# Kernel tuning notes

Hardware: AMD Instinct MI355X
Metric: run time of the kernel (lower is better)

## Reference

```python
import jax, jax.numpy as jnp
import numpy as np

B, C, L = 2, 512, 4096
HEADS, KV_HEADS, DIM_HEAD = 8, 2, 64
ROTARY_DIM = 32  # int(64 * 0.5), even
ROPE_THETA = 10000.0
SCALE = DIM_HEAD ** -0.5


def _rotate_half(x):
    # pairs (x0, x1) -> (-x1, x0), interleaved layout
    x = x.reshape(*x.shape[:-1], x.shape[-1] // 2, 2)
    x1, x2 = x[..., 0], x[..., 1]
    return jnp.stack([-x2, x1], axis=-1).reshape(*x.shape[:-2], x.shape[-2] * 2)


def _rope_sin_cos(seq_len, rotary_dim, theta, dtype):
    positions = jnp.arange(seq_len, dtype=dtype)
    half = rotary_dim // 2
    inv_freq = theta ** (-2.0 * jnp.arange(half, dtype=dtype) / rotary_dim)
    sinusoid = positions[:, None] * inv_freq[None, :]          # (L, half)
    sin = jnp.repeat(jnp.sin(sinusoid), 2, axis=-1)            # (L, rotary_dim) interleaved
    cos = jnp.repeat(jnp.cos(sinusoid), 2, axis=-1)
    return sin[None, None], cos[None, None]                    # (1,1,L,rotary_dim)


def setup_inputs() -> dict:
    key = jax.random.key(0)
    kx, kq, kkv, ko = jax.random.split(key, 4)
    s = 0.02
    return {
        "x": jax.random.normal(kx, (B, C, L), dtype=jnp.float32),
        "Wq": jax.random.normal(kq, (HEADS * DIM_HEAD, C), dtype=jnp.float32) * s,
        "Wkv": jax.random.normal(kkv, (2 * KV_HEADS * DIM_HEAD, C), dtype=jnp.float32) * s,
        "Wo": jax.random.normal(ko, (C, HEADS * DIM_HEAD), dtype=jnp.float32) * s,
    }


def reference(x, Wq, Wkv, Wo):
    b, c, l = x.shape
    x_t = jnp.swapaxes(x, 1, 2)                                 # (B, L, C)
    q = x_t @ Wq.T                                              # (B, L, H*dh)
    kv = x_t @ Wkv.T                                            # (B, L, KVH*2*dh)
    q = q.reshape(b, l, HEADS, DIM_HEAD).transpose(0, 2, 1, 3)  # (B, H, L, dh)
    kv = kv.reshape(b, l, KV_HEADS, 2 * DIM_HEAD).transpose(0, 2, 1, 3)
    k, v = jnp.split(kv, 2, axis=-1)                            # (B, KVH, L, dh) each

    sin, cos = _rope_sin_cos(l, ROTARY_DIM, ROPE_THETA, x.dtype)
    q_rot, q_pass = q[..., :ROTARY_DIM], q[..., ROTARY_DIM:]
    k_rot, k_pass = k[..., :ROTARY_DIM], k[..., ROTARY_DIM:]
    q_rot = q_rot * cos + _rotate_half(q_rot) * sin
    k_rot = k_rot * cos + _rotate_half(k_rot) * sin
    q = jnp.concatenate([q_rot, q_pass], axis=-1)
    k = jnp.concatenate([k_rot, k_pass], axis=-1)

    rep = HEADS // KV_HEADS
    k = jnp.repeat(k, rep, axis=1)                              # (B, H, L, dh)
    v = jnp.repeat(v, rep, axis=1)

    q = q * SCALE
    attn = jnp.einsum('bhid,bhjd->bhij', q, k)                  # (B, H, L, L)
    attn = jax.nn.softmax(attn, axis=-1)
    out = jnp.einsum('bhij,bhjd->bhid', attn, v)                # (B, H, L, dh)
    out = out.transpose(0, 2, 1, 3).reshape(b, l, HEADS * DIM_HEAD)
    out = out @ Wo.T                                            # (B, L, C)
    return jnp.swapaxes(out, 1, 2)                              # (B, C, L)
```

## Files before the change

kernel.cpp:

```cpp
#include <hip/hip_runtime.h>

using f16   = _Float16;
using f16x2 = __attribute__((ext_vector_type(2))) f16;
using f16x4 = __attribute__((ext_vector_type(4))) f16;
using f16x8 = __attribute__((ext_vector_type(8))) f16;
using f32x4 = __attribute__((ext_vector_type(4))) float;

#define L_ 4096
#define C_ 512

static __device__ __forceinline__ float fast_exp2(float x) {
#if __has_builtin(__builtin_amdgcn_exp2f)
  return __builtin_amdgcn_exp2f(x);
#else
  float r; asm("v_exp_f32 %0, %1" : "=v"(r) : "v"(x)); return r;
#endif
}

static __device__ __forceinline__ f16x2 pk2(float a, float b) {
  return __builtin_bit_cast(f16x2, __builtin_amdgcn_cvt_pkrtz(a, b));
}

static __device__ __forceinline__ void gl16(const char* g, char* l) {
  __builtin_amdgcn_global_load_lds(
      (const __attribute__((address_space(1))) unsigned int*)g,
      (__attribute__((address_space(3))) unsigned int*)l, 16, 0, 0);
}

#define WS_SC    0u
#define WS_WQKV  524288u
#define WS_WO    1310720u
#define WS_Q     1835008u
#define WS_K     10223616u
#define WS_VT    12320768u
#define WS_ATT   14417920u
#define WS_OP    22806528u
#define WS_LS2   56360960u
#define WS_END2  56885248u

__global__ __launch_bounds__(256) void prep_kernel(
    const float* __restrict__ Wq, const float* __restrict__ Wkv,
    const float* __restrict__ Wo,
    f16* __restrict__ wqkv, f16* __restrict__ wo16, float2* __restrict__ sc) {
  int t = blockIdx.x * 256 + threadIdx.x;
  if (t < 98304) {
    int idx = t * 4;
    float4 v = (idx < 262144) ? *(const float4*)(Wq + idx)
                              : *(const float4*)(Wkv + (idx - 262144));
    f16x4 o = {(f16)v.x, (f16)v.y, (f16)v.z, (f16)v.w};
    *(f16x4*)(wqkv + idx) = o;
  } else if (t < 163840) {
    int idx = (t - 98304) * 4;
    float4 v = *(const float4*)(Wo + idx);
    f16x4 o = {(f16)v.x, (f16)v.y, (f16)v.z, (f16)v.w};
    *(f16x4*)(wo16 + idx) = o;
  } else if (t < 229376) {
    int e = t - 163840;
    int l = e >> 4, p = e & 15;
    float invf = exp2f(-(float)p * (13.287712379549449f / 16.0f));
    float ang = (float)l * invf;
    sc[e] = make_float2(sinf(ang), cosf(ang));
  }
}

__global__ __launch_bounds__(256) void qkv_kernel(
    const float* __restrict__ x, const f16* __restrict__ wqkv,
    const float2* __restrict__ sc,
    f16* __restrict__ Qo, f16* __restrict__ Ko, f16* __restrict__ Vto) {
  __shared__ __align__(16) f16 xt[32 * 512];
  char* xl = (char*)xt;
  int bid = blockIdx.x;
  int b   = bid / 384;
  int rem = bid % 384;
  int ot  = rem >> 7;
  int lt  = rem & 127;
  int wave = threadIdx.x >> 6, lane = threadIdx.x & 63;
  int lo = lane & 15, hi = lane >> 4;
  int obase = ot * 256 + wave * 64;
  int lbase = lt * 32;
  const float* xb = x + (size_t)b * C_ * L_;

  {
    int l  = threadIdx.x & 31;
    int cg = threadIdx.x >> 5;
#pragma unroll
    for (int p = 0; p < 16; ++p) {
      int c4 = (p * 8 + cg) * 4;
      float v0 = xb[(size_t)(c4 + 0) * L_ + lbase + l];
      float v1 = xb[(size_t)(c4 + 1) * L_ + lbase + l];
      float v2 = xb[(size_t)(c4 + 2) * L_ + lbase + l];
      float v3 = xb[(size_t)(c4 + 3) * L_ + lbase + l];
      f16x2 p01 = pk2(v0, v1), p23 = pk2(v2, v3);
      f16x4 w = {p01[0], p01[1], p23[0], p23[1]};
      int col = (c4 * 2) ^ ((l & 7) * 16);
      *(f16x4*)(xl + l * 1024 + col) = w;
    }
  }
  __syncthreads();

  f32x4 acc[4][2] = {};
  for (int kc = 0; kc < 512; kc += 32) {
    f16x8 aw[4];
#pragma unroll
    for (int oc = 0; oc < 4; ++oc)
      aw[oc] = *(const f16x8*)(wqkv + (obase + oc * 16 + lo) * 512 + kc + hi * 8);
#pragma unroll
    for (int lc = 0; lc < 2; ++lc) {
      int row = lc * 16 + lo;
      f16x8 bx = *(const f16x8*)(xl + row * 1024 + (((kc + hi * 8) * 2) ^ ((row & 7) * 16)));
#pragma unroll
      for (int oc = 0; oc < 4; ++oc)
        acc[oc][lc] = __builtin_amdgcn_mfma_f32_16x16x32_f16(aw[oc], bx, acc[oc][lc], 0, 0, 0);
    }
  }

  bool is_q = obase < 512;
  int  og   = obase - 512;
  int  kvh  = is_q ? 0 : (og >> 7);
  bool is_v = (!is_q) && ((og & 127) == 64);
  int  h    = obase >> 6;
  const float QSCALE = 0.125f * 1.44269504088896340736f;

#pragma unroll
  for (int oc = 0; oc < 4; ++oc) {
#pragma unroll
    for (int lc = 0; lc < 2; ++lc) {
      f32x4 v = acc[oc][lc];
      int l = lbase + lc * 16 + lo;
      int d = oc * 16 + hi * 4;
      if (!is_v && oc < 2) {
        int p0 = d >> 1;
        float2 s0 = sc[l * 16 + p0];
        float2 s1 = sc[l * 16 + p0 + 1];
        float a0 = v[0], a1 = v[1], a2 = v[2], a3 = v[3];
        v[0] = a0 * s0.y - a1 * s0.x;
        v[1] = a1 * s0.y + a0 * s0.x;
        v[2] = a2 * s1.y - a3 * s1.x;
        v[3] = a3 * s1.y + a2 * s1.x;
      }
      if (is_q) {
        f16x4 st = {(f16)(v[0] * QSCALE), (f16)(v[1] * QSCALE),
                    (f16)(v[2] * QSCALE), (f16)(v[3] * QSCALE)};
        *(f16x4*)(Qo + (((size_t)b * 8 + h) * L_ + l) * 64 + d) = st;
      } else if (!is_v) {
        f16x4 st = {(f16)v[0], (f16)v[1], (f16)v[2], (f16)v[3]};
        int t = l >> 6, r = l & 63;
        int u = (d >> 3) ^ (r & 7);
        int w = (hi & 1) * 8;
        char* Kb = (char*)Ko + (size_t)(b * 2 + kvh) * (L_ * 128);
        *(f16x4*)(Kb + (size_t)t * 8192 + r * 128 + u * 16 + w) = st;
      } else {
        int t = l >> 6, kk = l & 63;
        int m = kk >> 3, i8 = kk & 7;
        int ca = (m >> 2) * 64 + ((2 * m) & 3) * 16 + ((m >> 1) & 1) * 8;
        int bcol = ca + (i8 < 4 ? 2 * i8 : 8 + 2 * i8);
        char* Vb = (char*)Vto + (size_t)(b * 2 + kvh) * (L_ * 128);
#pragma unroll
        for (int i = 0; i < 4; ++i) {
          int rv = d + i;
          *(f16*)(Vb + (size_t)t * 8192 + rv * 128 + (bcol ^ ((rv & 7) << 4))) = (f16)v[i];
        }
      }
    }
  }
}

template <int SPLIT>
__global__ __launch_bounds__(512) void attn_kernel(
    const f16* __restrict__ Qi, const f16* __restrict__ Ki,
    const f16* __restrict__ Vti, f16* __restrict__ att,
    f16* __restrict__ opart, float* __restrict__ lsews) {
  __shared__ __align__(16) char smem[2][16384];
  int bid  = blockIdx.x;
  int half = (SPLIT > 1) ? (bid >> 7) : 0;
  int rem7 = bid & 127;
  int b   = rem7 >> 6;
  int rr  = rem7 & 63;
  int h   = rr >> 3;
  int qt  = rr & 7;
  int tid  = threadIdx.x;
  int wave = tid >> 6, lane = tid & 63;
  int lo = lane & 15, hi = lane >> 4;
  int kvh = h >> 2;
  const f16*  Qp   = Qi + ((size_t)(b * 8 + h) * L_) * 64;
  const char* Ksrc = (const char*)Ki  + (size_t)(b * 2 + kvh) * (L_ * 128)
                     + (size_t)half * (L_ / SPLIT) * 128;
  const char* Vsrc = (const char*)Vti + (size_t)(b * 2 + kvh) * (L_ * 128)
                     + (size_t)half * (L_ / SPLIT) * 128;

  int lqb = qt * 512 + wave * 64;
  f16x8 qf[4][2];
#pragma unroll
  for (int qi = 0; qi < 4; ++qi)
#pragma unroll
    for (int hf = 0; hf < 2; ++hf)
      qf[qi][hf] = *(const f16x8*)(Qp + (size_t)(lqb + qi * 16 + lo) * 64 + hf * 32 + hi * 8);

  int c0 = tid;
#define STAGE(t, base_) do {                                           \
    gl16(Ksrc + (size_t)(t) * 8192 + c0 * 16, (char*)(base_) + c0 * 16); \
    gl16(Vsrc + (size_t)(t) * 8192 + c0 * 16, (char*)(base_) + 8192 + c0 * 16); \
  } while (0)

  f32x4 oacc[4][4] = {};
  f32x4 lse[4] = {};
  const f16x8 ones8 = {(f16)1.f, (f16)1.f, (f16)1.f, (f16)1.f,
                       (f16)1.f, (f16)1.f, (f16)1.f, (f16)1.f};
  int swz = (lo & 7) << 4;

#define COMPUTE(buf_) do {                                                          \
    const char* kb = (const char*)(buf_);                                           \
    const char* vb = kb + 8192;                                                     \
    _Pragma("unroll")                                                               \
    for (int jp = 0; jp < 2; ++jp) {                                                \
      f32x4 s[2][4] = {};                                                           \
      __builtin_amdgcn_s_setprio(1);                                                \
      _Pragma("unroll")                                                             \
      for (int jj = 0; jj < 2; ++jj) {                                              \
        int j = jp * 2 + jj;                                                        \
        f16x8 ka0 = *(const f16x8*)(kb + (j * 16 + lo) * 128 + ((hi * 16) ^ swz));  \
        f16x8 ka1 = *(const f16x8*)(kb + (j * 16 + lo) * 128 + ((64 + hi * 16) ^ swz)); \
        _Pragma("unroll")                                                           \
        for (int qi = 0; qi < 4; ++qi) {                                            \
          s[jj][qi] = __builtin_amdgcn_mfma_f32_16x16x32_f16(ka0, qf[qi][0], s[jj][qi], 0, 0, 0); \
          s[jj][qi] = __builtin_amdgcn_mfma_f32_16x16x32_f16(ka1, qf[qi][1], s[jj][qi], 0, 0, 0); \
        }                                                                           \
      }                                                                             \
      __builtin_amdgcn_s_setprio(0);                                                \
      f16x8 pc[4];                                                                  \
      _Pragma("unroll")                                                             \
      for (int qi = 0; qi < 4; ++qi) {                                              \
        f16x2 a0 = pk2(fast_exp2(s[0][qi][0]), fast_exp2(s[0][qi][1]));             \
        f16x2 a1 = pk2(fast_exp2(s[0][qi][2]), fast_exp2(s[0][qi][3]));             \
        f16x2 b0 = pk2(fast_exp2(s[1][qi][0]), fast_exp2(s[1][qi][1]));             \
        f16x2 b1 = pk2(fast_exp2(s[1][qi][2]), fast_exp2(s[1][qi][3]));             \
        f16x4 l4 = __builtin_shufflevector(a0, a1, 0, 1, 2, 3);                     \
        f16x4 h4 = __builtin_shufflevector(b0, b1, 0, 1, 2, 3);                     \
        pc[qi] = __builtin_shufflevector(l4, h4, 0, 1, 2, 3, 4, 5, 6, 7);           \
      }                                                                             \
      __builtin_amdgcn_s_setprio(1);                                                \
      _Pragma("unroll")                                                             \
      for (int dc = 0; dc < 4; ++dc) {                                              \
        f16x8 vv = *(const f16x8*)(vb + (dc * 16 + lo) * 128 + ((jp * 64 + hi * 16) ^ swz)); \
        _Pragma("unroll")                                                           \
        for (int qi = 0; qi < 4; ++qi)                                              \
          oacc[dc][qi] = __builtin_amdgcn_mfma_f32_16x16x32_f16(vv, pc[qi], oacc[dc][qi], 0, 0, 0); \
      }                                                                             \
      _Pragma("unroll")                                                             \
      for (int qi = 0; qi < 4; ++qi)                                                \
        lse[qi] = __builtin_amdgcn_mfma_f32_16x16x32_f16(ones8, pc[qi], lse[qi], 0, 0, 0); \
      __builtin_amdgcn_s_setprio(0);                                                \
    }                                                                               \
  } while (0)

  const int NT = 64 / SPLIT;
  STAGE(0, smem[0]);
  __syncthreads();

  for (int t = 0; t < NT; ++t) {
    if (t + 1 < NT) STAGE(t + 1, smem[(t + 1) & 1]);
    COMPUTE(smem[t & 1]);
    __syncthreads();
  }

#pragma unroll
  for (int qi = 0; qi < 4; ++qi) {
    int lq = lqb + qi * 16 + lo;
    if constexpr (SPLIT > 1) {
      size_t obase = (((size_t)(half * 2 + b) * 8 + h) * L_ + lq) * 64;
#pragma unroll
      for (int dc = 0; dc < 4; ++dc) {
        f16x4 st;
#pragma unroll
        for (int i = 0; i < 4; ++i) st[i] = (f16)oacc[dc][qi][i];
        *(f16x4*)(opart + obase + dc * 16 + hi * 4) = st;
      }
      if (hi == 0)
        lsews[((size_t)(half * 2 + b) * 8 + h) * L_ + lq] = lse[qi][0];
    } else {
      float inv = 1.f / lse[qi][0];
#pragma unroll
      for (int dc = 0; dc < 4; ++dc) {
        f16x4 st;
#pragma unroll
        for (int i = 0; i < 4; ++i) st[i] = (f16)(oacc[dc][qi][i] * inv);
        *(f16x4*)(att + ((size_t)b * L_ + lq) * 512 + h * 64 + dc * 16 + hi * 4) = st;
      }
    }
  }
#undef STAGE
#undef COMPUTE
}

template <int SPLIT>
__global__ __launch_bounds__(256) void combine_kernel(
    const f16* __restrict__ opart, const float* __restrict__ lsews,
    f16* __restrict__ att) {
  int t = blockIdx.x * 256 + threadIdx.x;
  int d4 = t & 15;
  int lq = (t >> 4) & 4095;
  int h  = (t >> 16) & 7;
  int b  = t >> 19;
  const size_t HS  = (size_t)2 * 8 * 4096 * 64;
  const size_t LSS = (size_t)2 * 8 * 4096;
  size_t base  = (((size_t)b * 8 + h) * 4096 + lq) * 64 + d4 * 4;
  size_t lbase = ((size_t)b * 8 + h) * 4096 + lq;
  float o[4] = {};
  float ls = 0.f;
#pragma unroll
  for (int s = 0; s < SPLIT; ++s) {
    f16x4 op = *(const f16x4*)(opart + s * HS + base);
#pragma unroll
    for (int i = 0; i < 4; ++i) o[i] += (float)op[i];
    ls += lsews[s * LSS + lbase];
  }
  float inv = 1.f / ls;
  f16x4 st;
#pragma unroll
  for (int i = 0; i < 4; ++i) st[i] = (f16)(o[i] * inv);
  *(f16x4*)(att + ((size_t)b * 4096 + lq) * 512 + h * 64 + d4 * 4) = st;
}

__global__ __launch_bounds__(256) void oproj_kernel(
    const f16* __restrict__ att, const f16* __restrict__ wo16,
    float* __restrict__ out) {
  int bid = blockIdx.x;
  int b   = bid / 256;
  int rem = bid % 256;
  int ct  = rem >> 7;
  int lt  = rem & 127;
  int wave = threadIdx.x >> 6, lane = threadIdx.x & 63;
  int lo = lane & 15, hi = lane >> 4;
  int cobase = ct * 256 + wave * 64;
  int lbase  = lt * 32;
  const f16* ab = att + (size_t)b * L_ * 512;

  f32x4 acc[4][2] = {};
  for (int kc = 0; kc < 512; kc += 32) {
    f16x8 aw[4];
#pragma unroll
    for (int cc = 0; cc < 4; ++cc)
      aw[cc] = *(const f16x8*)(wo16 + (cobase + cc * 16 + lo) * 512 + kc + hi * 8);
#pragma unroll
    for (int lc = 0; lc < 2; ++lc) {
      f16x8 bx = *(const f16x8*)(ab + (size_t)(lbase + lc * 16 + lo) * 512 + kc + hi * 8);
#pragma unroll
      for (int cc = 0; cc < 4; ++cc)
        acc[cc][lc] = __builtin_amdgcn_mfma_f32_16x16x32_f16(aw[cc], bx, acc[cc][lc], 0, 0, 0);
    }
  }
  float* ob = out + (size_t)b * C_ * L_;
#pragma unroll
  for (int cc = 0; cc < 4; ++cc)
#pragma unroll
    for (int lc = 0; lc < 2; ++lc) {
      int l = lbase + lc * 16 + lo;
#pragma unroll
      for (int i = 0; i < 4; ++i) {
        int co = cobase + cc * 16 + hi * 4 + i;
        ob[(size_t)co * L_ + l] = acc[cc][lc][i];
      }
    }
}

extern "C" void kernel_launch(void* const* d_in, const int* in_sizes, int n_in,
                              void* d_out, int out_size, void* d_ws, size_t ws_size,
                              hipStream_t stream) {
  const float* x   = (const float*)d_in[0];
  const float* Wq  = (const float*)d_in[1];
  const float* Wkv = (const float*)d_in[2];
  const float* Wo  = (const float*)d_in[3];
  char* ws = (char*)d_ws;
  float2* sc  = (float2*)(ws + WS_SC);
  f16* wqkv   = (f16*)(ws + WS_WQKV);
  f16* wo16   = (f16*)(ws + WS_WO);
  f16* Qb     = (f16*)(ws + WS_Q);
  f16* Kb     = (f16*)(ws + WS_K);
  f16* Vtb    = (f16*)(ws + WS_VT);
  f16* attb   = (f16*)(ws + WS_ATT);
  f16* opb    = (f16*)(ws + WS_OP);
  float* lsb  = (float*)(ws + WS_LS2);

  prep_kernel<<<1024, 256, 0, stream>>>(Wq, Wkv, Wo, wqkv, wo16, sc);
  qkv_kernel<<<768, 256, 0, stream>>>(x, wqkv, sc, Qb, Kb, Vtb);
  if (ws_size >= (size_t)WS_END2) {
    attn_kernel<2><<<256, 512, 0, stream>>>(Qb, Kb, Vtb, attb, opb, lsb);
    combine_kernel<2><<<4096, 256, 0, stream>>>(opb, lsb, attb);
  } else {
    attn_kernel<1><<<128, 512, 0, stream>>>(Qb, Kb, Vtb, attb, opb, lsb);
  }
  oproj_kernel<<<512, 256, 0, stream>>>(attb, wo16, (float*)d_out);
}
```

Baseline: 141.7 us.

## Fuse split-KV combine into output projection kernel

Replaces the separate combine kernel and output-projection kernel with one kernel. It merges the two attention partial outputs, normalises them by the summed LSE and stages the tile in swizzled LDS, then runs the Wo GEMM over both output-channel halves. This drops one launch and the write and reread of the intermediate attention buffer. In exchange each block now does the work of two projection tiles, so the grid halves to 256 blocks, and it uses 32KB of LDS per block, which may lower occupancy.

Measured after the change: 133.0 us. 1.07x faster.

```diff
diff --git a/kernel.cpp b/kernel.cpp
--- a/kernel.cpp
+++ b/kernel.cpp
@@ -292,33 +292,78 @@
 #undef COMPUTE
 }
 
-template <int SPLIT>
-__global__ __launch_bounds__(256) void combine_kernel(
+__global__ __launch_bounds__(256) void oproj_fused_kernel(
     const f16* __restrict__ opart, const float* __restrict__ lsews,
-    f16* __restrict__ att) {
-  int t = blockIdx.x * 256 + threadIdx.x;
-  int d4 = t & 15;
-  int lq = (t >> 4) & 4095;
-  int h  = (t >> 16) & 7;
-  int b  = t >> 19;
+    const f16* __restrict__ wo16, float* __restrict__ out) {
+  __shared__ __align__(16) f16 bt[32 * 512];
+  __shared__ float linv[32][8];
+  char* bl = (char*)bt;
+  int bid = blockIdx.x;
+  int b   = bid >> 7;
+  int lt  = bid & 127;
+  int lbase = lt * 32;
+  int tid  = threadIdx.x;
+  int wave = tid >> 6, lane = tid & 63;
+  int lo = lane & 15, hi = lane >> 4;
   const size_t HS  = (size_t)2 * 8 * 4096 * 64;
   const size_t LSS = (size_t)2 * 8 * 4096;
-  size_t base  = (((size_t)b * 8 + h) * 4096 + lq) * 64 + d4 * 4;
-  size_t lbase = ((size_t)b * 8 + h) * 4096 + lq;
-  float o[4] = {};
-  float ls = 0.f;
-#pragma unroll
-  for (int s = 0; s < SPLIT; ++s) {
-    f16x4 op = *(const f16x4*)(opart + s * HS + base);
-#pragma unroll
-    for (int i = 0; i < 4; ++i) o[i] += (float)op[i];
-    ls += lsews[s * LSS + lbase];
-  }
-  float inv = 1.f / ls;
-  f16x4 st;
-#pragma unroll
-  for (int i = 0; i < 4; ++i) st[i] = (f16)(o[i] * inv);
-  *(f16x4*)(att + ((size_t)b * 4096 + lq) * 512 + h * 64 + d4 * 4) = st;
+
+  {
+    int r = tid >> 3, h = tid & 7;
+    size_t lidx = ((size_t)b * 8 + h) * L_ + lbase + r;
+    linv[r][h] = 1.f / (lsews[lidx] + lsews[LSS + lidx]);
+  }
+  __syncthreads();
+
+#pragma unroll
+  for (int p = 0; p < 8; ++p) {
+    int idx = p * 256 + tid;
+    int r = idx >> 6, u = idx & 63;
+    int h = u >> 3, d = (u & 7) * 8;
+    size_t base = (((size_t)b * 8 + h) * L_ + lbase + r) * 64 + d;
+    f16x8 p0 = *(const f16x8*)(opart + base);
+    f16x8 p1 = *(const f16x8*)(opart + HS + base);
+    float iv = linv[r][h];
+    f16x2 c0 = pk2(((float)p0[0] + (float)p1[0]) * iv, ((float)p0[1] + (float)p1[1]) * iv);
+    f16x2 c1 = pk2(((float)p0[2] + (float)p1[2]) * iv, ((float)p0[3] + (float)p1[3]) * iv);
+    f16x2 c2 = pk2(((float)p0[4] + (float)p1[4]) * iv, ((float)p0[5] + (float)p1[5]) * iv);
+    f16x2 c3 = pk2(((float)p0[6] + (float)p1[6]) * iv, ((float)p0[7] + (float)p1[7]) * iv);
+    f16x8 w = {c0[0], c0[1], c1[0], c1[1], c2[0], c2[1], c3[0], c3[1]};
+    *(f16x8*)(bl + r * 1024 + ((u * 16) ^ ((r & 7) * 16))) = w;
+  }
+  __syncthreads();
+
+  float* ob = out + (size_t)b * C_ * L_;
+#pragma unroll
+  for (int ct = 0; ct < 2; ++ct) {
+    int cobase = ct * 256 + wave * 64;
+    f32x4 acc[4][2] = {};
+    for (int kc = 0; kc < 512; kc += 32) {
+      f16x8 aw[4];
+#pragma unroll
+      for (int cc = 0; cc < 4; ++cc)
+        aw[cc] = *(const f16x8*)(wo16 + (cobase + cc * 16 + lo) * 512 + kc + hi * 8);
+#pragma unroll
+      for (int lc = 0; lc < 2; ++lc) {
+        int row = lc * 16 + lo;
+        f16x8 bx = *(const f16x8*)(bl + row * 1024 + (((kc + hi * 8) * 2) ^ ((row & 7) * 16)));
+#pragma unroll
+        for (int cc = 0; cc < 4; ++cc)
+          acc[cc][lc] = __builtin_amdgcn_mfma_f32_16x16x32_f16(aw[cc], bx, acc[cc][lc], 0, 0, 0);
+      }
+    }
+#pragma unroll
+    for (int cc = 0; cc < 4; ++cc)
+#pragma unroll
+      for (int lc = 0; lc < 2; ++lc) {
+        int l = lbase + lc * 16 + lo;
+#pragma unroll
+        for (int i = 0; i < 4; ++i) {
+          int co = cobase + cc * 16 + hi * 4 + i;
+          ob[(size_t)co * L_ + l] = acc[cc][lc][i];
+        }
+      }
+  }
 }
 
 __global__ __launch_bounds__(256) void oproj_kernel(
@@ -385,9 +430,9 @@
   qkv_kernel<<<768, 256, 0, stream>>>(x, wqkv, sc, Qb, Kb, Vtb);
   if (ws_size >= (size_t)WS_END2) {
     attn_kernel<2><<<256, 512, 0, stream>>>(Qb, Kb, Vtb, attb, opb, lsb);
-    combine_kernel<2><<<4096, 256, 0, stream>>>(opb, lsb, attb);
+    oproj_fused_kernel<<<256, 256, 0, stream>>>(opb, lsb, wo16, (float*)d_out);
   } else {
     attn_kernel<1><<<128, 512, 0, stream>>>(Qb, Kb, Vtb, attb, opb, lsb);
-  }
-  oproj_kernel<<<512, 256, 0, stream>>>(attb, wo16, (float*)d_out);
-}
+    oproj_kernel<<<512, 256, 0, stream>>>(attb, wo16, (float*)d_out);
+  }
+}
```
